# Performance work log

Hardware: AMD Instinct MI355X
Metric: run time of the kernel (lower is better)

## Reference

```python
import math
import jax, jax.numpy as jnp
import numpy as np

B, N = 1, 512
C_S, C_Z, H, C, P_Q, P_V = 384, 128, 12, 16, 4, 8
CAT = C_Z * H + C * H + 3 * H * P_V + 1  # 2017


def _apply(t_r, t_t, x):
    # t_r: (b,n,3,3), t_t: (b,n,3), x: (b,3,h,p,n) -> global frame coords
    xg = jnp.einsum('bnij,bjhpn->bihpn', t_r, x)
    return xg + jnp.swapaxes(t_t, 1, 2)[:, :, None, None, :]


def setup_inputs() -> dict:
    key = jax.random.key(0)
    ks = jax.random.split(key, 14)
    f = lambda k, shp: jax.random.normal(k, shp, dtype=jnp.float32)
    return {
        's': f(ks[0], (B, C_S, N)),
        'z': f(ks[1], (B, C_Z, N, N)),
        't_r': f(ks[2], (B, N, 3, 3)),
        't_t': f(ks[3], (B, N, 3)),
        'Wq': f(ks[4], (C * H, C_S)) * 0.02,
        'Wk': f(ks[5], (C * H, C_S)) * 0.02,
        'Wv': f(ks[6], (C * H, C_S)) * 0.02,
        'Wqp': f(ks[7], (3 * H * P_Q, C_S)) * 0.02,
        'Wkp': f(ks[8], (3 * H * P_Q, C_S)) * 0.02,
        'Wvp': f(ks[9], (3 * H * P_V, C_S)) * 0.02,
        'Wb': f(ks[10], (H, C_Z)) * 0.02,
        'gamma': f(ks[11], (H, 1, 1)) * 0.5,
        'Ws': f(ks[12], (C_S, CAT)) * 0.02,
        'bs': jnp.zeros((C_S,), dtype=jnp.float32),
    }


def reference(s, z, t_r, t_t, Wq, Wk, Wv, Wqp, Wkp, Wvp, Wb, gamma, Ws, bs):
    b, _, n = s.shape
    w_c = math.sqrt(2.0 / (9.0 * P_Q))
    w_l = math.sqrt(1.0 / 3.0)

    proj = lambda W: jnp.einsum('oc,bcn->bon', W, s)
    # torch rearrange 'b (c h) i -> b c h i' == reshape(b, c, h, n)
    q = proj(Wq).reshape(b, C, H, n)
    k = proj(Wk).reshape(b, C, H, n)
    v = proj(Wv).reshape(b, C, H, n)
    qp = proj(Wqp).reshape(b, 3, H, P_Q, n)
    kp = proj(Wkp).reshape(b, 3, H, P_Q, n)
    vp = proj(Wvp).reshape(b, 3, H, P_V, n)

    qg = _apply(t_r, t_t, qp)  # (b,3,h,p,n)
    kg = _apply(t_r, t_t, kp)
    diff = qg[..., :, None] - kg[..., None, :]          # (b,3,h,p,n,n)
    dist2 = jnp.sum(diff * diff, axis=(1, 3))           # sum coords + points -> (b,h,n,n)
    tmp = jax.nn.softplus(gamma)[None] * (w_c / 2.0) * dist2

    b_bias = jnp.einsum('hc,bcij->bhij', Wb, z)
    qk = jnp.einsum('bchi,bchj->bhij', q, k) / math.sqrt(C)
    a = jax.nn.softmax(w_l * (qk + b_bias - tmp), axis=-1)  # (b,h,n,n)

    o1 = jnp.einsum('bhij,bcij->bchi', a, z).reshape(b, C_Z * H, n)
    o2 = jnp.einsum('bhij,bchj->bchi', a, v).reshape(b, C * H, n)

    vg = _apply(t_r, t_t, vp)                           # (b,3,h,pv,n)
    o3g = jnp.einsum('bhij,bchpj->bchpi', a, vg)        # (b,3,h,pv,n)
    t_r_inv = jnp.swapaxes(t_r, -1, -2)
    t_t_inv = jnp.einsum('bnij,bnj->bni', -t_r_inv, t_t)
    o3 = _apply(t_r_inv, t_t_inv, o3g).reshape(b, 3 * H * P_V, n)
    o3_norm = jnp.linalg.norm(o3, axis=1, keepdims=True)  # (b,1,n)

    cat = jnp.concatenate([o1, o2, o3, o3_norm], axis=1)  # (b, CAT, n)
    return jnp.einsum('oc,bcn->bon', Ws, cat) + bs[None, :, None]
```

## Files before the change

kernel.cpp:

```cpp
#include <hip/hip_runtime.h>
#include <math.h>

#define N 512
#define H 12
#define CC 16
#define CZ 128
#define CS 384
#define PQ 4
#define PV 8
#define CATR 2017

__global__ __launch_bounds__(256) void k_proj(
    const float* __restrict__ s,
    const float* __restrict__ Wq, const float* __restrict__ Wk, const float* __restrict__ Wv,
    const float* __restrict__ Wqp, const float* __restrict__ Wkp, const float* __restrict__ Wvp,
    float* __restrict__ proj)
{
    __shared__ float Wt[16][33];
    __shared__ float St[32][128];
    int t = threadIdx.x;
    int o0 = blockIdx.x * 16;
    int n0 = blockIdx.y * 128;
    const float* Wsrc; int orow;
    if (o0 < 192)      { Wsrc = Wq;  orow = o0; }
    else if (o0 < 384) { Wsrc = Wk;  orow = o0-192; }
    else if (o0 < 576) { Wsrc = Wv;  orow = o0-384; }
    else if (o0 < 720) { Wsrc = Wqp; orow = o0-576; }
    else if (o0 < 864) { Wsrc = Wkp; orow = o0-720; }
    else               { Wsrc = Wvp; orow = o0-864; }

    int og = t >> 6, nl = t & 63;
    float acc[4][2] = {};
    for (int c0 = 0; c0 < CS; c0 += 32) {
        __syncthreads();
        for (int k = 0; k < 2; k++) {
            int idx = t + k*256;
            int oo = idx >> 5, ccol = idx & 31;
            Wt[oo][ccol] = Wsrc[(orow+oo)*CS + c0 + ccol];
        }
        for (int k = 0; k < 4; k++) {
            int idx = t + k*256;
            int ccr = idx >> 5, nn4 = idx & 31;
            float4 v = *(const float4*)&s[(c0+ccr)*N + n0 + nn4*4];
            *(float4*)&St[ccr][nn4*4] = v;
        }
        __syncthreads();
        for (int kk = 0; kk < 32; kk++) {
            float sv0 = St[kk][nl], sv1 = St[kk][nl+64];
            #pragma unroll
            for (int r = 0; r < 4; r++) {
                float w = Wt[og*4+r][kk];
                acc[r][0] += w * sv0;
                acc[r][1] += w * sv1;
            }
        }
    }
    for (int r = 0; r < 4; r++) {
        int o = o0 + og*4 + r;
        proj[o*N + n0 + nl]      = acc[r][0];
        proj[o*N + n0 + 64 + nl] = acc[r][1];
    }
}

__global__ void k_frames(const float* __restrict__ proj,
                         const float* __restrict__ t_r, const float* __restrict__ t_t,
                         float* __restrict__ qg, float* __restrict__ kg, float* __restrict__ vg)
{
    int gid = blockIdx.x * blockDim.x + threadIdx.x;
    int n = gid & (N-1);
    int hp = gid >> 9;
    if (hp >= 192) return;
    const float* src; float* dst; int rowb, stride;
    if (hp < 48)      { src = proj + 576*N; dst = qg; rowb = hp;    stride = 48; }
    else if (hp < 96) { src = proj + 720*N; dst = kg; rowb = hp-48; stride = 48; }
    else              { src = proj + 864*N; dst = vg; rowb = hp-96; stride = 96; }
    float x0 = src[(rowb + 0*stride)*N + n];
    float x1 = src[(rowb + 1*stride)*N + n];
    float x2 = src[(rowb + 2*stride)*N + n];
    #pragma unroll
    for (int d = 0; d < 3; d++) {
        float r0 = t_r[(n*3+d)*3+0], r1 = t_r[(n*3+d)*3+1], r2 = t_r[(n*3+d)*3+2];
        dst[(rowb + d*stride)*N + n] = r0*x0 + r1*x1 + r2*x2 + t_t[n*3+d];
    }
}

__global__ void k_sq(const float* __restrict__ qg, const float* __restrict__ kg,
                     float* __restrict__ sq_q, float* __restrict__ sq_k)
{
    int gid = blockIdx.x * blockDim.x + threadIdx.x;
    int n = gid & (N-1);
    int sel = gid >> 9;
    int h = sel % H;
    const float* g = (sel < H) ? qg : kg;
    float* outp = (sel < H) ? sq_q : sq_k;
    float acc = 0.f;
    #pragma unroll
    for (int d = 0; d < 3; d++)
        #pragma unroll
        for (int p = 0; p < PQ; p++) {
            float v = g[(size_t)((d*H + h)*PQ + p)*N + n];
            acc += v*v;
        }
    outp[h*N + n] = acc;
}

__global__ __launch_bounds__(256) void k_attn(
    const float* __restrict__ z, const float* __restrict__ proj,
    const float* __restrict__ qg, const float* __restrict__ kg,
    const float* __restrict__ sq_q, const float* __restrict__ sq_k,
    const float* __restrict__ Wb, const float* __restrict__ gamma,
    float* __restrict__ a)
{
    __shared__ float redbuf[128*52];
    __shared__ float sred[2][H][2];
    int i = blockIdx.x;
    int t = threadIdx.x;
    int half = t >> 7;
    int jl = t & 127;
    int j4 = jl * 4;
    const float w_l  = 0.57735026918962584f;
    const float w_c2 = 0.11785113019775793f;

    float ch[H];
    #pragma unroll
    for (int h = 0; h < H; h++) {
        float g = gamma[h];
        float sp = (g > 20.f) ? g : log1pf(expf(g));
        ch[h] = sp * w_c2;
    }

    float acc[H][4] = {};

    {
        const float* zi = z + (size_t)i * N;
        int cbeg = half * 64;
        for (int c = cbeg; c < cbeg + 64; c += 4) {
            float4 z0 = *(const float4*)&zi[(size_t)(c+0)*N*N + j4];
            float4 z1 = *(const float4*)&zi[(size_t)(c+1)*N*N + j4];
            float4 z2 = *(const float4*)&zi[(size_t)(c+2)*N*N + j4];
            float4 z3 = *(const float4*)&zi[(size_t)(c+3)*N*N + j4];
            #pragma unroll
            for (int h = 0; h < H; h++) {
                float w0 = Wb[h*CZ + c+0], w1 = Wb[h*CZ + c+1];
                float w2 = Wb[h*CZ + c+2], w3 = Wb[h*CZ + c+3];
                acc[h][0] += w0*z0.x + w1*z1.x + w2*z2.x + w3*z3.x;
                acc[h][1] += w0*z0.y + w1*z1.y + w2*z2.y + w3*z3.y;
                acc[h][2] += w0*z0.z + w1*z1.z + w2*z2.z + w3*z3.z;
                acc[h][3] += w0*z0.w + w1*z1.w + w2*z2.w + w3*z3.w;
            }
        }
    }

    {
        const float* q = proj;
        const float* k = proj + 192*N;
        for (int c = half*8; c < half*8 + 8; c++) {
            #pragma unroll
            for (int h = 0; h < H; h++) {
                int r = c*H + h;
                float qv = 0.25f * q[(size_t)r*N + i];
                float4 k4 = *(const float4*)&k[(size_t)r*N + j4];
                acc[h][0] += qv*k4.x; acc[h][1] += qv*k4.y;
                acc[h][2] += qv*k4.z; acc[h][3] += qv*k4.w;
            }
        }
    }

    {
        for (int dp = half; dp < 12; dp += 2) {
            int d = dp >> 2, p = dp & 3;
            #pragma unroll
            for (int h = 0; h < H; h++) {
                int r = (d*H + h)*PQ + p;
                float qv = 2.f * ch[h] * qg[(size_t)r*N + i];
                float4 k4 = *(const float4*)&kg[(size_t)r*N + j4];
                acc[h][0] += qv*k4.x; acc[h][1] += qv*k4.y;
                acc[h][2] += qv*k4.z; acc[h][3] += qv*k4.w;
            }
        }
    }

    if (half == 1) {
        #pragma unroll
        for (int h = 0; h < H; h++)
            *(float4*)&redbuf[jl*52 + h*4] = *(float4*)&acc[h][0];
    }
    __syncthreads();
    if (half == 0) {
        #pragma unroll
        for (int h = 0; h < H; h++) {
            float4 o = *(const float4*)&redbuf[jl*52 + h*4];
            acc[h][0] += o.x; acc[h][1] += o.y; acc[h][2] += o.z; acc[h][3] += o.w;
        }
        #pragma unroll
        for (int h = 0; h < H; h++) {
            float s0 = sq_q[h*N + i];
            float4 sk = *(const float4*)&sq_k[h*N + j4];
            acc[h][0] = w_l*(acc[h][0] - ch[h]*(s0 + sk.x));
            acc[h][1] = w_l*(acc[h][1] - ch[h]*(s0 + sk.y));
            acc[h][2] = w_l*(acc[h][2] - ch[h]*(s0 + sk.z));
            acc[h][3] = w_l*(acc[h][3] - ch[h]*(s0 + sk.w));
        }
        int wv = t >> 6, lane = t & 63;
        #pragma unroll
        for (int h = 0; h < H; h++) {
            float m = fmaxf(fmaxf(acc[h][0], acc[h][1]), fmaxf(acc[h][2], acc[h][3]));
            for (int s = 32; s > 0; s >>= 1) m = fmaxf(m, __shfl_xor(m, s));
            if (lane == 0) sred[0][h][wv] = m;
        }
    }
    __syncthreads();
    if (half == 0) {
        int wv = t >> 6, lane = t & 63;
        #pragma unroll
        for (int h = 0; h < H; h++) {
            float m = fmaxf(sred[0][h][0], sred[0][h][1]);
            acc[h][0] = __expf(acc[h][0]-m); acc[h][1] = __expf(acc[h][1]-m);
            acc[h][2] = __expf(acc[h][2]-m); acc[h][3] = __expf(acc[h][3]-m);
            float sm = acc[h][0]+acc[h][1]+acc[h][2]+acc[h][3];
            for (int s = 32; s > 0; s >>= 1) sm += __shfl_xor(sm, s);
            if (lane == 0) sred[1][h][wv] = sm;
        }
    }
    __syncthreads();
    if (half == 0) {
        #pragma unroll
        for (int h = 0; h < H; h++) {
            float inv = 1.f / (sred[1][h][0] + sred[1][h][1]);
            float4 o;
            o.x = acc[h][0]*inv; o.y = acc[h][1]*inv;
            o.z = acc[h][2]*inv; o.w = acc[h][3]*inv;
            *(float4*)&a[((size_t)h*N + i)*N + j4] = o;
        }
    }
}

__global__ __launch_bounds__(256) void k_o1(
    const float* __restrict__ z, const float* __restrict__ a, float* __restrict__ cat)
{
    __shared__ float als[H*516];
    __shared__ float zls[128*68];
    int i = blockIdx.x;
    int t = threadIdx.x;
    int cg = t & 31, hg = (t>>5)&3, jh = t>>7;

    for (int k = 0; k < 6; k++) {
        int idx = t + k*256;
        int h = idx >> 7, jj4 = idx & 127;
        *(float4*)&als[h*516 + jj4*4] = *(const float4*)&a[((size_t)h*N + i)*N + jj4*4];
    }
    float acc[4][3] = {};
    for (int jc = 0; jc < 8; jc++) {
        __syncthreads();
        for (int k = 0; k < 8; k++) {
            int idx = t + k*256;
            int c = idx >> 4, j4 = idx & 15;
            *(float4*)&zls[c*68 + j4*4] =
                *(const float4*)&z[((size_t)c*N + i)*N + jc*64 + j4*4];
        }
        __syncthreads();
        int jb = jh * 32;
        #pragma unroll
        for (int s = 0; s < 8; s++) {
            int jo = jb + s*4;
            float4 a0 = *(const float4*)&als[(hg*3+0)*516 + jc*64 + jo];
            float4 a1 = *(const float4*)&als[(hg*3+1)*516 + jc*64 + jo];
            float4 a2 = *(const float4*)&als[(hg*3+2)*516 + jc*64 + jo];
            #pragma unroll
            for (int r = 0; r < 4; r++) {
                float4 zz = *(const float4*)&zls[(cg + 32*r)*68 + jo];
                acc[r][0] += zz.x*a0.x + zz.y*a0.y + zz.z*a0.z + zz.w*a0.w;
                acc[r][1] += zz.x*a1.x + zz.y*a1.y + zz.z*a1.z + zz.w*a1.w;
                acc[r][2] += zz.x*a2.x + zz.y*a2.y + zz.z*a2.z + zz.w*a2.w;
            }
        }
    }
    __syncthreads();
    if (jh == 1) {
        float* rb = zls + (t & 127)*13;
        #pragma unroll
        for (int r = 0; r < 4; r++)
            #pragma unroll
            for (int hh = 0; hh < 3; hh++) rb[r*3+hh] = acc[r][hh];
    }
    __syncthreads();
    if (jh == 0) {
        const float* rb = zls + t*13;
        #pragma unroll
        for (int r = 0; r < 4; r++)
            #pragma unroll
            for (int hh = 0; hh < 3; hh++) acc[r][hh] += rb[r*3+hh];
        #pragma unroll
        for (int r = 0; r < 4; r++)
            #pragma unroll
            for (int hh = 0; hh < 3; hh++) {
                int c = cg + 32*r, h = hg*3 + hh;
                cat[(size_t)(c*H + h)*N + i] = acc[r][hh];
            }
    }
}

__global__ __launch_bounds__(256) void k_o2o3g(
    const float* __restrict__ a, const float* __restrict__ proj, const float* __restrict__ vg,
    float* __restrict__ cat, float* __restrict__ o3g)
{
    __shared__ float ats[16*132];
    __shared__ float vts[40*132];
    int h = blockIdx.x, i0 = blockIdx.y*16;
    int t = threadIdx.x;
    int il = t & 15, rg = (t>>4)&7, jh = t>>7;
    const float* v = proj + 384*N;
    float acc[5] = {};
    for (int jc = 0; jc < 4; jc++) {
        __syncthreads();
        for (int k = 0; k < 2; k++) {
            int idx = t + k*256;
            int ii = idx >> 5, j4 = idx & 31;
            *(float4*)&ats[ii*132 + j4*4] =
                *(const float4*)&a[((size_t)h*N + i0+ii)*N + jc*128 + j4*4];
        }
        for (int idx = t; idx < 1280; idx += 256) {
            int r = idx >> 5, j4 = idx & 31;
            const float* src = (r < 16) ? (v + (size_t)(r*H + h)*N)
                : (vg + (size_t)(((r-16)>>3)*96 + h*PV + ((r-16)&7))*N);
            *(float4*)&vts[r*132 + j4*4] = *(const float4*)&src[jc*128 + j4*4];
        }
        __syncthreads();
        int jb = jh * 64;
        #pragma unroll
        for (int s = 0; s < 16; s++) {
            int jo = jb + s*4;
            float4 a4 = *(const float4*)&ats[il*132 + jo];
            #pragma unroll
            for (int r = 0; r < 5; r++) {
                float4 v4 = *(const float4*)&vts[(rg*5+r)*132 + jo];
                acc[r] += v4.x*a4.x + v4.y*a4.y + v4.z*a4.z + v4.w*a4.w;
            }
        }
    }
    __syncthreads();
    if (jh == 1) {
        float* rb = ats + (t & 127)*6;
        #pragma unroll
        for (int r = 0; r < 5; r++) rb[r] = acc[r];
    }
    __syncthreads();
    if (jh == 0) {
        const float* rb = ats + t*6;
        #pragma unroll
        for (int r = 0; r < 5; r++) acc[r] += rb[r];
        #pragma unroll
        for (int r = 0; r < 5; r++) {
            int row = rg*5 + r;
            if (row < 16) cat[(size_t)(1536 + row*H + h)*N + i0 + il] = acc[r];
            else { int rr = row - 16;
                   o3g[(size_t)((rr>>3)*96 + h*PV + (rr&7))*N + i0 + il] = acc[r]; }
        }
    }
}

__global__ void k_o3(const float* __restrict__ o3g,
                     const float* __restrict__ t_r, const float* __restrict__ t_t,
                     float* __restrict__ cat)
{
    int gid = blockIdx.x*blockDim.x + threadIdx.x;
    int i = gid & (N-1), hp = gid >> 9;
    if (hp >= 96) return;
    float x0 = o3g[(size_t)(0*96 + hp)*N + i] - t_t[i*3+0];
    float x1 = o3g[(size_t)(1*96 + hp)*N + i] - t_t[i*3+1];
    float x2 = o3g[(size_t)(2*96 + hp)*N + i] - t_t[i*3+2];
    #pragma unroll
    for (int d = 0; d < 3; d++) {
        float o = t_r[(i*3+0)*3+d]*x0 + t_r[(i*3+1)*3+d]*x1 + t_r[(i*3+2)*3+d]*x2;
        cat[(size_t)(1728 + d*96 + hp)*N + i] = o;
    }
}

__global__ void k_norm(float* __restrict__ cat)
{
    int i = blockIdx.x*blockDim.x + threadIdx.x;
    if (i >= N) return;
    float acc = 0.f;
    for (int r = 0; r < 288; r++) {
        float v = cat[(size_t)(1728+r)*N + i];
        acc += v*v;
    }
    cat[(size_t)2016*N + i] = sqrtf(acc);
}

__global__ __launch_bounds__(256) void k_final(
    const float* __restrict__ Ws, const float* __restrict__ bs,
    const float* __restrict__ cat, float* __restrict__ out)
{
    __shared__ float Wt[16*33];
    __shared__ float Ct[32*66];
    int o0 = blockIdx.x*16, n0 = blockIdx.y*64;
    int ks = blockIdx.z;
    int kbeg = ks*505, kend = min(CATR, kbeg+505);
    int t = threadIdx.x;
    int og = t >> 6, nl = t & 63;
    float acc[4] = {};
    for (int c0 = kbeg; c0 < kend; c0 += 32) {
        __syncthreads();
        for (int k = 0; k < 2; k++) {
            int idx = t + k*256;
            int oo = idx >> 5, ccol = idx & 31;
            int c = c0 + ccol;
            Wt[oo*33 + ccol] = (c < kend) ? Ws[(size_t)(o0+oo)*CATR + c] : 0.f;
        }
        for (int k = 0; k < 4; k++) {
            int idx = t + k*256;
            int ccr = idx >> 5, j2 = idx & 31;
            int c = c0 + ccr;
            float2 vv; vv.x = 0.f; vv.y = 0.f;
            if (c < kend) vv = *(const float2*)&cat[(size_t)c*N + n0 + j2*2];
            *(float2*)&Ct[ccr*66 + j2*2] = vv;
        }
        __syncthreads();
        int klim = min(32, kend - c0);
        for (int kk = 0; kk < klim; kk++) {
            float cv = Ct[kk*66 + nl];
            #pragma unroll
            for (int r = 0; r < 4; r++)
                acc[r] += Wt[(og*4+r)*33 + kk] * cv;
        }
    }
    #pragma unroll
    for (int r = 0; r < 4; r++) {
        int o = o0 + og*4 + r;
        float val = acc[r];
        if (ks == 0) val += bs[o];
        atomicAdd(&out[(size_t)o*N + n0 + nl], val);
    }
}

extern "C" void kernel_launch(void* const* d_in, const int* in_sizes, int n_in,
                              void* d_out, int out_size, void* d_ws, size_t ws_size,
                              hipStream_t stream)
{
    const float* s     = (const float*)d_in[0];
    const float* z     = (const float*)d_in[1];
    const float* t_r   = (const float*)d_in[2];
    const float* t_t   = (const float*)d_in[3];
    const float* Wq    = (const float*)d_in[4];
    const float* Wk    = (const float*)d_in[5];
    const float* Wv    = (const float*)d_in[6];
    const float* Wqp   = (const float*)d_in[7];
    const float* Wkp   = (const float*)d_in[8];
    const float* Wvp   = (const float*)d_in[9];
    const float* Wb    = (const float*)d_in[10];
    const float* gamma = (const float*)d_in[11];
    const float* Ws    = (const float*)d_in[12];
    const float* bs    = (const float*)d_in[13];
    float* out = (float*)d_out;

    float* ws   = (float*)d_ws;
    float* proj = ws;
    float* qg   = proj + 1152*N;
    float* kg   = qg   + 144*N;
    float* vg   = kg   + 144*N;
    float* sq_q = vg   + 288*N;
    float* sq_k = sq_q + H*N;
    float* o3g  = sq_k + H*N;
    float* a    = o3g  + 288*N;
    float* cat  = a    + (size_t)H*N*N;

    k_proj  <<<dim3(72,4),  256, 0, stream>>>(s, Wq, Wk, Wv, Wqp, Wkp, Wvp, proj);
    k_frames<<<384,         256, 0, stream>>>(proj, t_r, t_t, qg, kg, vg);
    k_sq    <<<48,          256, 0, stream>>>(qg, kg, sq_q, sq_k);
    k_attn  <<<512,         256, 0, stream>>>(z, proj, qg, kg, sq_q, sq_k, Wb, gamma, a);
    k_o1    <<<512,         256, 0, stream>>>(z, a, cat);
    k_o2o3g <<<dim3(12,32), 256, 0, stream>>>(a, proj, vg, cat, o3g);
    k_o3    <<<192,         256, 0, stream>>>(o3g, t_r, t_t, cat);
    k_norm  <<<2,           256, 0, stream>>>(cat);
    hipMemsetAsync(out, 0, (size_t)CS*N*sizeof(float), stream);
    k_final <<<dim3(24,8,4),256, 0, stream>>>(Ws, bs, cat, out);
}
```

Baseline: 416.4 us.

## Split attention into logits and softmax kernels, add more parallelism across blocks

The fused attention kernel becomes a logits kernel gridded over (i, j-chunk) with four channel groups per block, followed by a separate row softmax kernel. k_o1 is split over two channel halves and k_o2o3g uses smaller i tiles, which doubles the grids and changes the j-reduction to four ways. The goal is more blocks and better memory parallelism on the large z reads. The cost is an extra full read and write of the 12x512x512 attention tensor and an added launch.

```diff
diff --git a/kernel.cpp b/kernel.cpp
--- a/kernel.cpp
+++ b/kernel.cpp
@@ -104,198 +104,220 @@
     outp[h*N + n] = acc;
 }
 
-__global__ __launch_bounds__(256) void k_attn(
+__global__ __launch_bounds__(256) void k_logits(
     const float* __restrict__ z, const float* __restrict__ proj,
     const float* __restrict__ qg, const float* __restrict__ kg,
     const float* __restrict__ sq_q, const float* __restrict__ sq_k,
     const float* __restrict__ Wb, const float* __restrict__ gamma,
     float* __restrict__ a)
 {
-    __shared__ float redbuf[128*52];
-    __shared__ float sred[2][H][2];
+    __shared__ float red[12*2*256];
     int i = blockIdx.x;
+    int jc = blockIdx.y;
     int t = threadIdx.x;
-    int half = t >> 7;
-    int jl = t & 127;
-    int j4 = jl * 4;
+    int jl = t & 63;
+    int cgu = __builtin_amdgcn_readfirstlane(t >> 6);
+    int j = jc*256 + jl*4;
+    const size_t NN = (size_t)N*N;
     const float w_l  = 0.57735026918962584f;
     const float w_c2 = 0.11785113019775793f;
 
-    float ch[H];
+    float ch[12];
     #pragma unroll
-    for (int h = 0; h < H; h++) {
+    for (int h = 0; h < 12; h++) {
         float g = gamma[h];
         float sp = (g > 20.f) ? g : log1pf(expf(g));
         ch[h] = sp * w_c2;
     }
 
-    float acc[H][4] = {};
+    float acc[12][4] = {};
 
     {
-        const float* zi = z + (size_t)i * N;
-        int cbeg = half * 64;
-        for (int c = cbeg; c < cbeg + 64; c += 4) {
-            float4 z0 = *(const float4*)&zi[(size_t)(c+0)*N*N + j4];
-            float4 z1 = *(const float4*)&zi[(size_t)(c+1)*N*N + j4];
-            float4 z2 = *(const float4*)&zi[(size_t)(c+2)*N*N + j4];
-            float4 z3 = *(const float4*)&zi[(size_t)(c+3)*N*N + j4];
-            #pragma unroll
-            for (int h = 0; h < H; h++) {
-                float w0 = Wb[h*CZ + c+0], w1 = Wb[h*CZ + c+1];
-                float w2 = Wb[h*CZ + c+2], w3 = Wb[h*CZ + c+3];
-                acc[h][0] += w0*z0.x + w1*z1.x + w2*z2.x + w3*z3.x;
-                acc[h][1] += w0*z0.y + w1*z1.y + w2*z2.y + w3*z3.y;
-                acc[h][2] += w0*z0.z + w1*z1.z + w2*z2.z + w3*z3.z;
-                acc[h][3] += w0*z0.w + w1*z1.w + w2*z2.w + w3*z3.w;
-            }
-        }
-    }
-
+        const float* zp = z + (size_t)(cgu*32)*NN + (size_t)i*N + j;
+        for (int cc = 0; cc < 32; cc += 8) {
+            float4 zb[8];
+            #pragma unroll
+            for (int u = 0; u < 8; u++)
+                zb[u] = *(const float4*)(zp + (size_t)(cc+u)*NN);
+            #pragma unroll
+            for (int u = 0; u < 8; u++) {
+                int c = cgu*32 + cc + u;
+                #pragma unroll
+                for (int h = 0; h < 12; h++) {
+                    float w = Wb[h*CZ + c];
+                    acc[h][0] += w*zb[u].x; acc[h][1] += w*zb[u].y;
+                    acc[h][2] += w*zb[u].z; acc[h][3] += w*zb[u].w;
+                }
+            }
+        }
+    }
     {
-        const float* q = proj;
-        const float* k = proj + 192*N;
-        for (int c = half*8; c < half*8 + 8; c++) {
-            #pragma unroll
-            for (int h = 0; h < H; h++) {
-                int r = c*H + h;
+        const float* q  = proj;
+        const float* kk = proj + 192*N;
+        #pragma unroll
+        for (int cc = 0; cc < 4; cc++) {
+            int c = cgu*4 + cc;
+            #pragma unroll
+            for (int h = 0; h < 12; h++) {
+                int r = c*12 + h;
                 float qv = 0.25f * q[(size_t)r*N + i];
-                float4 k4 = *(const float4*)&k[(size_t)r*N + j4];
+                float4 k4 = *(const float4*)&kk[(size_t)r*N + j];
                 acc[h][0] += qv*k4.x; acc[h][1] += qv*k4.y;
                 acc[h][2] += qv*k4.z; acc[h][3] += qv*k4.w;
             }
         }
     }
-
     {
-        for (int dp = half; dp < 12; dp += 2) {
-            int d = dp >> 2, p = dp & 3;
-            #pragma unroll
-            for (int h = 0; h < H; h++) {
-                int r = (d*H + h)*PQ + p;
+        #pragma unroll
+        for (int dd = 0; dd < 3; dd++) {
+            int dp = cgu*3 + dd; int d = dp >> 2, p = dp & 3;
+            #pragma unroll
+            for (int h = 0; h < 12; h++) {
+                int r = (d*12 + h)*4 + p;
                 float qv = 2.f * ch[h] * qg[(size_t)r*N + i];
-                float4 k4 = *(const float4*)&kg[(size_t)r*N + j4];
+                float4 k4 = *(const float4*)&kg[(size_t)r*N + j];
                 acc[h][0] += qv*k4.x; acc[h][1] += qv*k4.y;
                 acc[h][2] += qv*k4.z; acc[h][3] += qv*k4.w;
             }
         }
     }
 
-    if (half == 1) {
-        #pragma unroll
-        for (int h = 0; h < H; h++)
-            *(float4*)&redbuf[jl*52 + h*4] = *(float4*)&acc[h][0];
-    }
-    __syncthreads();
-    if (half == 0) {
-        #pragma unroll
-        for (int h = 0; h < H; h++) {
-            float4 o = *(const float4*)&redbuf[jl*52 + h*4];
+    if (cgu >= 2) {
+        #pragma unroll
+        for (int h = 0; h < 12; h++) {
+            float4 v; v.x=acc[h][0]; v.y=acc[h][1]; v.z=acc[h][2]; v.w=acc[h][3];
+            *(float4*)&red[(h*2 + (cgu-2))*256 + jl*4] = v;
+        }
+    }
+    __syncthreads();
+    if (cgu < 2) {
+        #pragma unroll
+        for (int h = 0; h < 12; h++) {
+            float4 o = *(const float4*)&red[(h*2 + cgu)*256 + jl*4];
             acc[h][0] += o.x; acc[h][1] += o.y; acc[h][2] += o.z; acc[h][3] += o.w;
         }
-        #pragma unroll
-        for (int h = 0; h < H; h++) {
+        if (cgu == 1) {
+            #pragma unroll
+            for (int h = 0; h < 12; h++) {
+                float4 v; v.x=acc[h][0]; v.y=acc[h][1]; v.z=acc[h][2]; v.w=acc[h][3];
+                *(float4*)&red[(h*2 + 1)*256 + jl*4] = v;
+            }
+        }
+    }
+    __syncthreads();
+    if (cgu == 0) {
+        #pragma unroll
+        for (int h = 0; h < 12; h++) {
+            float4 o = *(const float4*)&red[(h*2 + 1)*256 + jl*4];
             float s0 = sq_q[h*N + i];
-            float4 sk = *(const float4*)&sq_k[h*N + j4];
-            acc[h][0] = w_l*(acc[h][0] - ch[h]*(s0 + sk.x));
-            acc[h][1] = w_l*(acc[h][1] - ch[h]*(s0 + sk.y));
-            acc[h][2] = w_l*(acc[h][2] - ch[h]*(s0 + sk.z));
-            acc[h][3] = w_l*(acc[h][3] - ch[h]*(s0 + sk.w));
-        }
-        int wv = t >> 6, lane = t & 63;
-        #pragma unroll
-        for (int h = 0; h < H; h++) {
-            float m = fmaxf(fmaxf(acc[h][0], acc[h][1]), fmaxf(acc[h][2], acc[h][3]));
-            for (int s = 32; s > 0; s >>= 1) m = fmaxf(m, __shfl_xor(m, s));
-            if (lane == 0) sred[0][h][wv] = m;
-        }
-    }
-    __syncthreads();
-    if (half == 0) {
-        int wv = t >> 6, lane = t & 63;
-        #pragma unroll
-        for (int h = 0; h < H; h++) {
-            float m = fmaxf(sred[0][h][0], sred[0][h][1]);
-            acc[h][0] = __expf(acc[h][0]-m); acc[h][1] = __expf(acc[h][1]-m);
-            acc[h][2] = __expf(acc[h][2]-m); acc[h][3] = __expf(acc[h][3]-m);
-            float sm = acc[h][0]+acc[h][1]+acc[h][2]+acc[h][3];
-            for (int s = 32; s > 0; s >>= 1) sm += __shfl_xor(sm, s);
-            if (lane == 0) sred[1][h][wv] = sm;
-        }
-    }
-    __syncthreads();
-    if (half == 0) {
-        #pragma unroll
-        for (int h = 0; h < H; h++) {
-            float inv = 1.f / (sred[1][h][0] + sred[1][h][1]);
-            float4 o;
-            o.x = acc[h][0]*inv; o.y = acc[h][1]*inv;
-            o.z = acc[h][2]*inv; o.w = acc[h][3]*inv;
-            *(float4*)&a[((size_t)h*N + i)*N + j4] = o;
-        }
-    }
+            float4 sk = *(const float4*)&sq_k[h*N + j];
+            float4 r;
+            r.x = w_l*(acc[h][0] + o.x - ch[h]*(s0 + sk.x));
+            r.y = w_l*(acc[h][1] + o.y - ch[h]*(s0 + sk.y));
+            r.z = w_l*(acc[h][2] + o.z - ch[h]*(s0 + sk.z));
+            r.w = w_l*(acc[h][3] + o.w - ch[h]*(s0 + sk.w));
+            *(float4*)&a[((size_t)h*N + i)*N + j] = r;
+        }
+    }
+}
+
+__global__ __launch_bounds__(256) void k_softmax(float* __restrict__ a)
+{
+    int r = blockIdx.x*4 + (threadIdx.x >> 6);
+    int l = threadIdx.x & 63;
+    float* row = a + (size_t)r*N + l*8;
+    float4 v0 = *(const float4*)row;
+    float4 v1 = *(const float4*)(row + 4);
+    float m = fmaxf(fmaxf(fmaxf(v0.x,v0.y),fmaxf(v0.z,v0.w)),
+                    fmaxf(fmaxf(v1.x,v1.y),fmaxf(v1.z,v1.w)));
+    for (int s = 32; s > 0; s >>= 1) m = fmaxf(m, __shfl_xor(m, s));
+    v0.x = __expf(v0.x-m); v0.y = __expf(v0.y-m);
+    v0.z = __expf(v0.z-m); v0.w = __expf(v0.w-m);
+    v1.x = __expf(v1.x-m); v1.y = __expf(v1.y-m);
+    v1.z = __expf(v1.z-m); v1.w = __expf(v1.w-m);
+    float sm = v0.x+v0.y+v0.z+v0.w+v1.x+v1.y+v1.z+v1.w;
+    for (int s = 32; s > 0; s >>= 1) sm += __shfl_xor(sm, s);
+    float inv = 1.f/sm;
+    v0.x*=inv; v0.y*=inv; v0.z*=inv; v0.w*=inv;
+    v1.x*=inv; v1.y*=inv; v1.z*=inv; v1.w*=inv;
+    *(float4*)row = v0;
+    *(float4*)(row+4) = v1;
 }
 
 __global__ __launch_bounds__(256) void k_o1(
     const float* __restrict__ z, const float* __restrict__ a, float* __restrict__ cat)
 {
-    __shared__ float als[H*516];
-    __shared__ float zls[128*68];
+    __shared__ float als[12*516];
+    __shared__ float zls[64*68];
     int i = blockIdx.x;
+    int c0 = blockIdx.y * 64;
     int t = threadIdx.x;
-    int cg = t & 31, hg = (t>>5)&3, jh = t>>7;
-
+    int cg = t & 31, hg = (t>>5)&1, jq = t>>6;
+
+    #pragma unroll
     for (int k = 0; k < 6; k++) {
         int idx = t + k*256;
-        int h = idx >> 7, jj4 = idx & 127;
-        *(float4*)&als[h*516 + jj4*4] = *(const float4*)&a[((size_t)h*N + i)*N + jj4*4];
-    }
-    float acc[4][3] = {};
+        int h = idx >> 7, j4 = idx & 127;
+        *(float4*)&als[h*516 + j4*4] = *(const float4*)&a[((size_t)h*N + i)*N + j4*4];
+    }
+    float acc[2][6] = {};
     for (int jc = 0; jc < 8; jc++) {
         __syncthreads();
-        for (int k = 0; k < 8; k++) {
+        #pragma unroll
+        for (int k = 0; k < 4; k++) {
             int idx = t + k*256;
             int c = idx >> 4, j4 = idx & 15;
             *(float4*)&zls[c*68 + j4*4] =
-                *(const float4*)&z[((size_t)c*N + i)*N + jc*64 + j4*4];
-        }
-        __syncthreads();
-        int jb = jh * 32;
-        #pragma unroll
-        for (int s = 0; s < 8; s++) {
-            int jo = jb + s*4;
-            float4 a0 = *(const float4*)&als[(hg*3+0)*516 + jc*64 + jo];
-            float4 a1 = *(const float4*)&als[(hg*3+1)*516 + jc*64 + jo];
-            float4 a2 = *(const float4*)&als[(hg*3+2)*516 + jc*64 + jo];
-            #pragma unroll
-            for (int r = 0; r < 4; r++) {
-                float4 zz = *(const float4*)&zls[(cg + 32*r)*68 + jo];
-                acc[r][0] += zz.x*a0.x + zz.y*a0.y + zz.z*a0.z + zz.w*a0.w;
-                acc[r][1] += zz.x*a1.x + zz.y*a1.y + zz.z*a1.z + zz.w*a1.w;
-                acc[r][2] += zz.x*a2.x + zz.y*a2.y + zz.z*a2.z + zz.w*a2.w;
-            }
-        }
-    }
-    __syncthreads();
-    if (jh == 1) {
-        float* rb = zls + (t & 127)*13;
-        #pragma unroll
-        for (int r = 0; r < 4; r++)
-            #pragma unroll
-            for (int hh = 0; hh < 3; hh++) rb[r*3+hh] = acc[r][hh];
-    }
-    __syncthreads();
-    if (jh == 0) {
-        const float* rb = zls + t*13;
-        #pragma unroll
-        for (int r = 0; r < 4; r++)
-            #pragma unroll
-            for (int hh = 0; hh < 3; hh++) acc[r][hh] += rb[r*3+hh];
-        #pragma unroll
-        for (int r = 0; r < 4; r++)
-            #pragma unroll
-            for (int hh = 0; hh < 3; hh++) {
-                int c = cg + 32*r, h = hg*3 + hh;
-                cat[(size_t)(c*H + h)*N + i] = acc[r][hh];
+                *(const float4*)&z[((size_t)(c0+c)*N + i)*N + jc*64 + j4*4];
+        }
+        __syncthreads();
+        #pragma unroll
+        for (int s = 0; s < 4; s++) {
+            int jo = jq*16 + s*4;
+            float4 z0 = *(const float4*)&zls[cg*68 + jo];
+            float4 z1 = *(const float4*)&zls[(cg+32)*68 + jo];
+            #pragma unroll
+            for (int hh = 0; hh < 6; hh++) {
+                float4 a4 = *(const float4*)&als[(hg*6+hh)*516 + jc*64 + jo];
+                acc[0][hh] += z0.x*a4.x + z0.y*a4.y + z0.z*a4.z + z0.w*a4.w;
+                acc[1][hh] += z1.x*a4.x + z1.y*a4.y + z1.z*a4.z + z1.w*a4.w;
+            }
+        }
+    }
+    __syncthreads();
+    if (jq >= 2) {
+        float* rb = &zls[((jq-2)*128 + (t & 127))*13];
+        #pragma unroll
+        for (int r = 0; r < 2; r++)
+            #pragma unroll
+            for (int hh = 0; hh < 6; hh++) rb[r*6+hh] = acc[r][hh];
+    }
+    __syncthreads();
+    if (jq < 2) {
+        const float* rb = &zls[(jq*128 + (t & 127))*13];
+        #pragma unroll
+        for (int r = 0; r < 2; r++)
+            #pragma unroll
+            for (int hh = 0; hh < 6; hh++) acc[r][hh] += rb[r*6+hh];
+        if (jq == 1) {
+            float* rb2 = &als[(t & 63)*13];
+            #pragma unroll
+            for (int r = 0; r < 2; r++)
+                #pragma unroll
+                for (int hh = 0; hh < 6; hh++) rb2[r*6+hh] = acc[r][hh];
+        }
+    }
+    __syncthreads();
+    if (jq == 0) {
+        const float* rb2 = &als[t*13];
+        #pragma unroll
+        for (int r = 0; r < 2; r++)
+            #pragma unroll
+            for (int hh = 0; hh < 6; hh++) {
+                float v = acc[r][hh] + rb2[r*6+hh];
+                int c = c0 + cg + 32*r;
+                int h = hg*6 + hh;
+                cat[(size_t)(c*H + h)*N + i] = v;
             }
     }
 }
@@ -304,32 +326,32 @@
     const float* __restrict__ a, const float* __restrict__ proj, const float* __restrict__ vg,
     float* __restrict__ cat, float* __restrict__ o3g)
 {
-    __shared__ float ats[16*132];
+    __shared__ float ats[8*132];
     __shared__ float vts[40*132];
-    int h = blockIdx.x, i0 = blockIdx.y*16;
+    int h = blockIdx.x, i0 = blockIdx.y*8;
     int t = threadIdx.x;
-    int il = t & 15, rg = (t>>4)&7, jh = t>>7;
+    int il = t & 7, rg = (t>>3)&7, jq = t>>6;
     const float* v = proj + 384*N;
     float acc[5] = {};
     for (int jc = 0; jc < 4; jc++) {
         __syncthreads();
-        for (int k = 0; k < 2; k++) {
-            int idx = t + k*256;
-            int ii = idx >> 5, j4 = idx & 31;
+        {
+            int ii = t >> 5, j4 = t & 31;
             *(float4*)&ats[ii*132 + j4*4] =
                 *(const float4*)&a[((size_t)h*N + i0+ii)*N + jc*128 + j4*4];
         }
-        for (int idx = t; idx < 1280; idx += 256) {
+        #pragma unroll
+        for (int k = 0; k < 5; k++) {
+            int idx = t + k*256;
             int r = idx >> 5, j4 = idx & 31;
             const float* src = (r < 16) ? (v + (size_t)(r*H + h)*N)
                 : (vg + (size_t)(((r-16)>>3)*96 + h*PV + ((r-16)&7))*N);
             *(float4*)&vts[r*132 + j4*4] = *(const float4*)&src[jc*128 + j4*4];
         }
         __syncthreads();
-        int jb = jh * 64;
-        #pragma unroll
-        for (int s = 0; s < 16; s++) {
-            int jo = jb + s*4;
+        #pragma unroll
+        for (int s = 0; s < 8; s++) {
+            int jo = jq*32 + s*4;
             float4 a4 = *(const float4*)&ats[il*132 + jo];
             #pragma unroll
             for (int r = 0; r < 5; r++) {
@@ -339,22 +361,32 @@
         }
     }
     __syncthreads();
-    if (jh == 1) {
-        float* rb = ats + (t & 127)*6;
+    if (jq >= 2) {
+        float* rb = &ats[((jq-2)*64 + (t & 63))*5];
         #pragma unroll
         for (int r = 0; r < 5; r++) rb[r] = acc[r];
     }
     __syncthreads();
-    if (jh == 0) {
-        const float* rb = ats + t*6;
+    if (jq < 2) {
+        const float* rb = &ats[(jq*64 + (t & 63))*5];
         #pragma unroll
         for (int r = 0; r < 5; r++) acc[r] += rb[r];
+        if (jq == 1) {
+            float* rb2 = &ats[640 + (t & 63)*5];
+            #pragma unroll
+            for (int r = 0; r < 5; r++) rb2[r] = acc[r];
+        }
+    }
+    __syncthreads();
+    if (jq == 0) {
+        const float* rb2 = &ats[640 + t*5];
         #pragma unroll
         for (int r = 0; r < 5; r++) {
+            float val = acc[r] + rb2[r];
             int row = rg*5 + r;
-            if (row < 16) cat[(size_t)(1536 + row*H + h)*N + i0 + il] = acc[r];
+            if (row < 16) cat[(size_t)(1536 + row*H + h)*N + i0 + il] = val;
             else { int rr = row - 16;
-                   o3g[(size_t)((rr>>3)*96 + h*PV + (rr&7))*N + i0 + il] = acc[r]; }
+                   o3g[(size_t)((rr>>3)*96 + h*PV + (rr&7))*N + i0 + il] = val; }
         }
     }
 }
@@ -465,14 +497,15 @@
     float* a    = o3g  + 288*N;
     float* cat  = a    + (size_t)H*N*N;
 
-    k_proj  <<<dim3(72,4),  256, 0, stream>>>(s, Wq, Wk, Wv, Wqp, Wkp, Wvp, proj);
-    k_frames<<<384,         256, 0, stream>>>(proj, t_r, t_t, qg, kg, vg);
-    k_sq    <<<48,          256, 0, stream>>>(qg, kg, sq_q, sq_k);
-    k_attn  <<<512,         256, 0, stream>>>(z, proj, qg, kg, sq_q, sq_k, Wb, gamma, a);
-    k_o1    <<<512,         256, 0, stream>>>(z, a, cat);
-    k_o2o3g <<<dim3(12,32), 256, 0, stream>>>(a, proj, vg, cat, o3g);
-    k_o3    <<<192,         256, 0, stream>>>(o3g, t_r, t_t, cat);
-    k_norm  <<<2,           256, 0, stream>>>(cat);
+    k_proj   <<<dim3(72,4),   256, 0, stream>>>(s, Wq, Wk, Wv, Wqp, Wkp, Wvp, proj);
+    k_frames <<<384,          256, 0, stream>>>(proj, t_r, t_t, qg, kg, vg);
+    k_sq     <<<48,           256, 0, stream>>>(qg, kg, sq_q, sq_k);
+    k_logits <<<dim3(512,2),  256, 0, stream>>>(z, proj, qg, kg, sq_q, sq_k, Wb, gamma, a);
+    k_softmax<<<1536,         256, 0, stream>>>(a);
+    k_o1     <<<dim3(512,2),  256, 0, stream>>>(z, a, cat);
+    k_o2o3g  <<<dim3(12,64),  256, 0, stream>>>(a, proj, vg, cat, o3g);
+    k_o3     <<<192,          256, 0, stream>>>(o3g, t_r, t_t, cat);
+    k_norm   <<<2,            256, 0, stream>>>(cat);
     hipMemsetAsync(out, 0, (size_t)CS*N*sizeof(float), stream);
-    k_final <<<dim3(24,8,4),256, 0, stream>>>(Ws, bs, cat, out);
-}
+    k_final  <<<dim3(24,8,4), 256, 0, stream>>>(Ws, bs, cat, out);
+}
```

New measurement: 418.2 us. About the same (+0.4%).
